# Optimization experiments

Hardware: AMD Instinct MI355X
Metric: run time of the kernel (lower is better)

Reference implementation:

```python
import jax, jax.numpy as jnp
import numpy as np

N, H, F, E, K = 4096, 512, 2048, 8, 2  # tokens, hidden, ffn(=4H), experts, top_k


def setup_inputs() -> dict:
    key = jax.random.key(0)
    ks = jax.random.split(key, 7)
    def w(k, shape, fan_in):
        return jax.random.normal(k, shape, dtype=jnp.float32) * (fan_in ** -0.5)
    return {
        "x": jax.random.normal(ks[0], (N, H), dtype=jnp.float32),
        "W_in": w(ks[1], (H, H), H),          # input_proj.weight  [out,in]
        "W_router": w(ks[2], (E, H), H),      # router.gate.weight [E,H]
        "W_gate": w(ks[3], (E, F, H), H),     # per-expert gate_proj.weight
        "W_up": w(ks[4], (E, F, H), H),       # per-expert up_proj.weight
        "W_down": w(ks[5], (E, H, F), F),     # per-expert down_proj.weight
        "W_out": w(ks[6], (H, H), H),         # output_proj.weight
    }


def reference(x, W_in, W_router, W_gate, W_up, W_down, W_out):
    h = x @ W_in.T                                  # [N,H] input_proj
    logits = h @ W_router.T                         # [N,E]
    # route_mode='balanced' and world_size==1 -> expert_bias is None
    probs = jax.nn.softmax(logits, axis=-1)
    top_w, top_i = jax.lax.top_k(probs, K)          # [N,K]
    top_w = jax.nn.softmax(top_w, axis=-1)          # renormalize over top-k

    # per-token combine weight for each expert: [N,E]
    onehot = jax.nn.one_hot(top_i, E, dtype=h.dtype)      # [N,K,E]
    combine_w = jnp.einsum('nk,nke->ne', top_w, onehot)

    def expert(wg, wu, wd):
        # SwiGLU FFN: down( silu(gate(h)) * up(h) )
        return (jax.nn.silu(h @ wg.T) * (h @ wu.T)) @ wd.T  # [N,H]

    expert_out = jax.vmap(expert)(W_gate, W_up, W_down)     # [E,N,H]
    combined = jnp.einsum('ne,enh->nh', combine_w, expert_out)
    return combined @ W_out.T                                # output_proj
```

## Files before the change

kernel.cpp:

```cpp
#include <hip/hip_runtime.h>
#include <hip/hip_bf16.h>

typedef unsigned short u16;
typedef unsigned int u32;
typedef short bf16x8 __attribute__((ext_vector_type(8)));
typedef float f32x4 __attribute__((ext_vector_type(4)));

#define AS1 __attribute__((address_space(1)))
#define AS3 __attribute__((address_space(3)))

#define NTOK 4096
#define HDIM 512
#define FDIM 2048
#define NEXP 8
#define NASSIGN (NTOK * 2)
#define NPAD (NASSIGN + NEXP * 128)
#define RBMAX 128

__device__ __forceinline__ void g2l16(const void* g, void* l) {
  __builtin_amdgcn_global_load_lds((const AS1 u32*)g, (AS3 u32*)l, 16, 0, 0);
}
__device__ __forceinline__ u16 f2bf(float f) {
  u32 u = __float_as_uint(f);
  u = (u + 0x7FFFu + ((u >> 16) & 1u)) >> 16;
  return (u16)u;
}
__device__ __forceinline__ float bf2f(u16 h) { return __uint_as_float(((u32)h) << 16); }
__device__ __forceinline__ u32 pkbf(float a, float b) {
  __hip_bfloat162 h = __float22bfloat162_rn(float2{a, b});
  u32 r;
  __builtin_memcpy(&r, &h, 4);
  return r;
}
__device__ __forceinline__ int4 pk8(const float4 a, const float4 b) {
  int4 r;
  r.x = (int)pkbf(a.x, a.y); r.y = (int)pkbf(a.z, a.w);
  r.z = (int)pkbf(b.x, b.y); r.w = (int)pkbf(b.z, b.w);
  return r;
}

#define WAITV6() asm volatile("s_waitcnt vmcnt(6)" ::: "memory")
#define WAITV4() asm volatile("s_waitcnt vmcnt(4)" ::: "memory")
#define WAITV2() asm volatile("s_waitcnt vmcnt(2)" ::: "memory")
#define WAITV0() asm volatile("s_waitcnt vmcnt(0)" ::: "memory")
#define LGKM0() asm volatile("s_waitcnt lgkmcnt(0)" ::: "memory")
#define BAR() __builtin_amdgcn_s_barrier()
#define SCB() __builtin_amdgcn_sched_barrier(0)
#define PRIO1() __builtin_amdgcn_s_setprio(1)
#define PRIO0() __builtin_amdgcn_s_setprio(0)
#define VMBAR() do { WAITV0(); BAR(); } while (0)

__global__ __launch_bounds__(256) void cvtall_kernel(
    const float* __restrict__ x, const float* __restrict__ Wi, const float* __restrict__ Wo,
    const float* __restrict__ Wg, const float* __restrict__ Wu, const float* __restrict__ Wd,
    u16* __restrict__ xb, u16* __restrict__ Wib, u16* __restrict__ Wob,
    u16* __restrict__ Wgb, u16* __restrict__ Wub, u16* __restrict__ Wdb) {
  const int c = blockIdx.x, tid = threadIdx.x;
  const float* s; u16* d; int cs;
  if (c < 128) { s = x; d = xb; cs = 0; }
  else if (c < 144) { s = Wi; d = Wib; cs = 128; }
  else if (c < 160) { s = Wo; d = Wob; cs = 144; }
  else if (c < 672) { s = Wg; d = Wgb; cs = 160; }
  else if (c < 1184) { s = Wu; d = Wub; cs = 672; }
  else { s = Wd; d = Wdb; cs = 1184; }
  const size_t base = (size_t)(c - cs) * 16384 + (size_t)tid * 8;
  const float* sp = s + base;
  u16* dp = d + base;
  float4 a[16];
#pragma unroll
  for (int j = 0; j < 8; ++j) {
    a[2 * j] = *(const float4*)(sp + j * 2048);
    a[2 * j + 1] = *(const float4*)(sp + j * 2048 + 4);
  }
#pragma unroll
  for (int j = 0; j < 8; ++j)
    *(int4*)(dp + j * 2048) = pk8(a[2 * j], a[2 * j + 1]);
}

__global__ __launch_bounds__(256) void wreff_kernel(
    const float* __restrict__ Wr, const float* __restrict__ Wi, double* __restrict__ wre) {
  const int t = blockIdx.x * 256 + threadIdx.x;
  const int e = t >> 9, k = t & 511;
  const float* wr = Wr + e * HDIM;
  double a0 = 0.0, a1 = 0.0, a2 = 0.0, a3 = 0.0;
  for (int j = 0; j < HDIM; j += 4) {
    a0 += (double)wr[j + 0] * (double)Wi[(j + 0) * HDIM + k];
    a1 += (double)wr[j + 1] * (double)Wi[(j + 1) * HDIM + k];
    a2 += (double)wr[j + 2] * (double)Wi[(j + 2) * HDIM + k];
    a3 += (double)wr[j + 3] * (double)Wi[(j + 3) * HDIM + k];
  }
  wre[t] = (a0 + a1) + (a2 + a3);
}

__global__ __launch_bounds__(128) void router_kernel(
    const float* __restrict__ x, const double* __restrict__ wre,
    int* __restrict__ idx, float* __restrict__ wts) {
  __shared__ double lw[NEXP * HDIM];
  for (int i = threadIdx.x; i < NEXP * HDIM; i += 128) lw[i] = wre[i];
  __syncthreads();
  const int n = blockIdx.x * 128 + threadIdx.x;
  const float* xr = x + (size_t)n * HDIM;
  double acc[NEXP] = {};
  for (int k4 = 0; k4 < HDIM / 4; ++k4) {
    const float4 xv = ((const float4*)xr)[k4];
    const float xc[4] = {xv.x, xv.y, xv.z, xv.w};
#pragma unroll
    for (int c = 0; c < 4; ++c) {
      const double xd = (double)xc[c];
#pragma unroll
      for (int e = 0; e < NEXP; ++e) acc[e] += xd * lw[e * HDIM + k4 * 4 + c];
    }
  }
  double mx = acc[0];
#pragma unroll
  for (int e = 1; e < NEXP; ++e) mx = acc[e] > mx ? acc[e] : mx;
  double p[NEXP], se = 0.0;
#pragma unroll
  for (int e = 0; e < NEXP; ++e) { p[e] = exp(acc[e] - mx); se += p[e]; }
  const double inv = 1.0 / se;
#pragma unroll
  for (int e = 0; e < NEXP; ++e) p[e] *= inv;
  int i0 = 0; double b0 = p[0];
#pragma unroll
  for (int e = 1; e < NEXP; ++e) if (p[e] > b0) { b0 = p[e]; i0 = e; }
  int i1 = -1; double b1 = -1.0;
#pragma unroll
  for (int e = 0; e < NEXP; ++e) if (e != i0 && p[e] > b1) { b1 = p[e]; i1 = e; }
  const double e0 = exp(b0), e1 = exp(b1);
  idx[2 * n] = i0; idx[2 * n + 1] = i1;
  wts[2 * n] = (float)(e0 / (e0 + e1));
  wts[2 * n + 1] = (float)(e1 / (e0 + e1));
}

__global__ void assign_kernel(const int* __restrict__ idx, int* __restrict__ tok,
                              int* __restrict__ pos, int* __restrict__ rbe,
                              int* __restrict__ rbp, int* __restrict__ nrb) {
  __shared__ int cnt[NEXP], cur[NEXP];
  const int tid = threadIdx.x;
  if (tid < NEXP) cnt[tid] = 0;
  __syncthreads();
  for (int a = tid; a < NASSIGN; a += 256) atomicAdd(&cnt[idx[a]], 1);
  __syncthreads();
  if (tid == 0) {
    int o = 0, n = 0;
    for (int e = 0; e < NEXP; ++e) {
      cur[e] = o;
      const int nb = (cnt[e] + 127) >> 7;
      for (int i = 0; i < nb; ++i) { rbe[n] = e; rbp[n] = o + i * 128; ++n; }
      o += nb * 128;
    }
    nrb[0] = n;
  }
  __syncthreads();
  for (int p = tid; p < NPAD; p += 256) tok[p] = 0;
  __syncthreads();
  for (int a = tid; a < NASSIGN; a += 256) {
    const int e = idx[a];
    const int q = atomicAdd(&cur[e], 1);
    tok[q] = a >> 1;
    pos[a] = q;
  }
}

template <int SB, int NT>
__device__ __forceinline__ void gemm128_body(
    const u16* __restrict__ A, const u16* __restrict__ B, void* __restrict__ C,
    int m0, int n0, int N, int K, u16* sm, int tid) {
  u16 *lA0 = sm, *lA1 = sm + 8192, *lB0 = sm + 16384, *lB1 = sm + 24576;
  const int w = tid >> 6, l = tid & 63;
  const int wm = (w >> 2) * 64, wn = (w & 3) * 32;
  const int lm = l & 15, lk = (l >> 4) * 8, xr = (l & 7) << 3;
  const int sr = l >> 3, sc = ((l & 7) ^ sr) * 8;
  const u16* As = A + (size_t)(m0 + w * 8 + sr) * K + sc;
  const u16* Bs = B + (size_t)(n0 + w * 8 + sr) * K + sc;
  f32x4 acc[4][2] = {};
  auto STG = [&](u16* dA, u16* dB, int kt) {
    g2l16(As + kt, dA + w * 512);
    g2l16(As + (size_t)64 * K + kt, dA + 4096 + w * 512);
    g2l16(Bs + kt, dB + w * 512);
    g2l16(Bs + (size_t)64 * K + kt, dB + 4096 + w * 512);
  };
  auto CMP = [&](const u16* a_, const u16* b_) {
#pragma unroll
    for (int kk = 0; kk < 2; ++kk) {
      const int ko = (kk * 32 + lk) ^ xr;
      bf16x8 af[4], bf[2];
#pragma unroll
      for (int i = 0; i < 4; ++i) af[i] = *(const bf16x8*)(a_ + (wm + i * 16 + lm) * 64 + ko);
#pragma unroll
      for (int j = 0; j < 2; ++j) bf[j] = *(const bf16x8*)(b_ + (wn + j * 16 + lm) * 64 + ko);
      PRIO1();
#pragma unroll
      for (int i = 0; i < 4; ++i)
#pragma unroll
        for (int j = 0; j < 2; ++j)
          acc[i][j] = __builtin_amdgcn_mfma_f32_16x16x32_bf16(af[i], bf[j], acc[i][j], 0, 0, 0);
      PRIO0();
    }
  };
  STG(lA0, lB0, 0);
  VMBAR();
  for (int t = 0; t < NT; t += 2) {
    if (t + 1 < NT) STG(lA1, lB1, (t + 1) * 64);
    CMP(lA0, lB0);
    VMBAR();
    if (t + 2 < NT) STG(lA0, lB0, (t + 2) * 64);
    CMP(lA1, lB1);
    VMBAR();
  }
  const int cr = (l >> 4) * 4, cc = lm;
#pragma unroll
  for (int i = 0; i < 4; ++i)
#pragma unroll
    for (int j = 0; j < 2; ++j)
#pragma unroll
      for (int r = 0; r < 4; ++r) {
        const size_t o = (size_t)(m0 + wm + i * 16 + cr + r) * N + n0 + wn + j * 16 + cc;
        if (SB) ((u16*)C)[o] = f2bf(acc[i][j][r]);
        else ((float*)C)[o] = acc[i][j][r];
      }
}

__global__ __launch_bounds__(512, 2) void ingemm_kernel(
    const u16* __restrict__ xb, const u16* __restrict__ Wib, u16* __restrict__ hb) {
  __shared__ __align__(16) u16 sm[32768];
  gemm128_body<1, 8>(xb, Wib, hb, blockIdx.y * 128, blockIdx.x * 128, HDIM, HDIM, sm, threadIdx.x);
}

__global__ __launch_bounds__(512, 2) void outgemm_kernel(
    const u16* __restrict__ dwn, const u16* __restrict__ Wob, const int* __restrict__ pos,
    const float* __restrict__ wts, float* __restrict__ out) {
  __shared__ __align__(16) u16 sm[32768];
  const int m0 = blockIdx.y * 128, n0 = blockIdx.x * 128;
  const int tid = threadIdx.x, w = tid >> 6, l = tid & 63;
  const int wm = (w >> 2) * 64, wn = (w & 3) * 32;
  const int lm = l & 15, lk = (l >> 4) * 8, xr = (l & 7) << 3;
  const int lr = l >> 3, c8 = l & 7;
  const int sc = (c8 ^ lr) * 8;
  const int t0 = m0 + w * 8 + lr, t1 = t0 + 64;
  const int p00 = pos[2 * t0], p01 = pos[2 * t0 + 1];
  const int p10 = pos[2 * t1], p11 = pos[2 * t1 + 1];
  const float w00 = wts[2 * t0], w01 = wts[2 * t0 + 1];
  const float w10 = wts[2 * t1], w11 = wts[2 * t1 + 1];
  const u16* A00 = dwn + (size_t)p00 * HDIM + c8 * 8;
  const u16* A01 = dwn + (size_t)p01 * HDIM + c8 * 8;
  const u16* A10 = dwn + (size_t)p10 * HDIM + c8 * 8;
  const u16* A11 = dwn + (size_t)p11 * HDIM + c8 * 8;
  const u16* Bs = Wob + (size_t)(n0 + w * 8 + lr) * HDIM + sc;
  f32x4 acc[4][2] = {};
  bf16x8 a00, a01, a10, a11;
  auto ALOAD = [&](int kt) {
    a00 = *(const bf16x8*)(A00 + kt); a01 = *(const bf16x8*)(A01 + kt);
    a10 = *(const bf16x8*)(A10 + kt); a11 = *(const bf16x8*)(A11 + kt);
  };
  auto AWRITE = [&](u16* st) {
    bf16x8 r0, r1;
#pragma unroll
    for (int q = 0; q < 8; ++q) {
      r0[q] = (short)f2bf(w00 * bf2f((u16)a00[q]) + w01 * bf2f((u16)a01[q]));
      r1[q] = (short)f2bf(w10 * bf2f((u16)a10[q]) + w11 * bf2f((u16)a11[q]));
    }
    *(bf16x8*)(st + (w * 8 + lr) * 64 + sc) = r0;
    *(bf16x8*)(st + (64 + w * 8 + lr) * 64 + sc) = r1;
  };
  auto STGB = [&](u16* st, int kt) {
    g2l16(Bs + kt, st + 8192 + w * 512);
    g2l16(Bs + (size_t)64 * HDIM + kt, st + 8192 + 4096 + w * 512);
  };
  auto CMP = [&](const u16* a_, const u16* b_) {
#pragma unroll
    for (int kk = 0; kk < 2; ++kk) {
      const int ko = (kk * 32 + lk) ^ xr;
      bf16x8 af[4], bf[2];
#pragma unroll
      for (int i = 0; i < 4; ++i) af[i] = *(const bf16x8*)(a_ + (wm + i * 16 + lm) * 64 + ko);
#pragma unroll
      for (int j = 0; j < 2; ++j) bf[j] = *(const bf16x8*)(b_ + (wn + j * 16 + lm) * 64 + ko);
      PRIO1();
#pragma unroll
      for (int i = 0; i < 4; ++i)
#pragma unroll
        for (int j = 0; j < 2; ++j)
          acc[i][j] = __builtin_amdgcn_mfma_f32_16x16x32_bf16(af[i], bf[j], acc[i][j], 0, 0, 0);
      PRIO0();
    }
  };
  ALOAD(0); SCB(); STGB(sm, 0);
  WAITV2(); AWRITE(sm);
  WAITV0(); LGKM0(); BAR(); SCB();
  for (int t = 0; t < 8; ++t) {
    u16* bu = sm + (t & 1) * 16384;
    u16* bn = sm + ((t + 1) & 1) * 16384;
    if (t < 7) { ALOAD((t + 1) * 64); SCB(); STGB(bn, (t + 1) * 64); }
    CMP(bu, bu + 8192);
    if (t < 7) { WAITV2(); AWRITE(bn); WAITV0(); }
    LGKM0(); BAR(); SCB();
  }
  const int cr = (l >> 4) * 4, cc = lm;
#pragma unroll
  for (int i = 0; i < 4; ++i)
#pragma unroll
    for (int j = 0; j < 2; ++j)
#pragma unroll
      for (int r = 0; r < 4; ++r)
        out[(size_t)(m0 + wm + i * 16 + cr + r) * HDIM + n0 + wn + j * 16 + cc] = acc[i][j][r];
}

__global__ __launch_bounds__(512, 2) void gateup_kernel(
    const u16* __restrict__ hb, const u16* __restrict__ Wg, const u16* __restrict__ Wu,
    u16* __restrict__ act, const int* __restrict__ tok, const int* __restrict__ rbe,
    const int* __restrict__ rbp, const int* __restrict__ nrb) {
  const int rb = blockIdx.y;
  if (rb >= nrb[0]) return;
  __shared__ __align__(16) u16 sm[73728];
  const int e = rbe[rb], p0 = rbp[rb], n0 = blockIdx.x * 128;
  const int tid = threadIdx.x, w = tid >> 6, l = tid & 63;
  const int wm = (w >> 2) * 64, wn = (w & 3) * 32;
  const int lm = l & 15, lk = (l >> 4) * 8, xr = (l & 7) << 3;
  const int sr = l >> 3, sc = ((l & 7) ^ sr) * 8;
  const u16* A0 = hb + (size_t)tok[p0 + w * 8 + sr] * HDIM + sc;
  const u16* A1 = hb + (size_t)tok[p0 + 64 + w * 8 + sr] * HDIM + sc;
  const u16* G0 = Wg + (size_t)e * FDIM * HDIM + (size_t)(n0 + w * 8 + sr) * HDIM + sc;
  const u16* G1 = G0 + (size_t)64 * HDIM;
  const u16* U0 = Wu + (size_t)e * FDIM * HDIM + (size_t)(n0 + w * 8 + sr) * HDIM + sc;
  const u16* U1 = U0 + (size_t)64 * HDIM;
  f32x4 ag[4][2] = {}, au[4][2] = {};
  auto STG = [&](int b, int kt) {
    u16* d = sm + b * 24576;
    g2l16(A0 + kt, d + w * 512);
    g2l16(A1 + kt, d + 4096 + w * 512);
    g2l16(G0 + kt, d + 8192 + w * 512);
    g2l16(G1 + kt, d + 12288 + w * 512);
    g2l16(U0 + kt, d + 16384 + w * 512);
    g2l16(U1 + kt, d + 20480 + w * 512);
  };
  auto CMP = [&](int b) {
    const u16* a_ = sm + b * 24576;
    const u16* g_ = a_ + 8192;
    const u16* u_ = a_ + 16384;
#pragma unroll
    for (int kk = 0; kk < 2; ++kk) {
      const int ko = (kk * 32 + lk) ^ xr;
      bf16x8 af[4], gf[2], uf[2];
#pragma unroll
      for (int i = 0; i < 4; ++i) af[i] = *(const bf16x8*)(a_ + (wm + i * 16 + lm) * 64 + ko);
#pragma unroll
      for (int j = 0; j < 2; ++j) {
        gf[j] = *(const bf16x8*)(g_ + (wn + j * 16 + lm) * 64 + ko);
        uf[j] = *(const bf16x8*)(u_ + (wn + j * 16 + lm) * 64 + ko);
      }
#pragma unroll
      for (int i = 0; i < 4; ++i)
#pragma unroll
        for (int j = 0; j < 2; ++j) {
          ag[i][j] = __builtin_amdgcn_mfma_f32_16x16x32_bf16(af[i], gf[j], ag[i][j], 0, 0, 0);
          au[i][j] = __builtin_amdgcn_mfma_f32_16x16x32_bf16(af[i], uf[j], au[i][j], 0, 0, 0);
        }
    }
  };
  STG(0, 0); STG(1, 64);
  WAITV6(); BAR();
#pragma unroll
  for (int t = 0; t < 8; ++t) {
    if (t + 2 < 8) STG((t + 2) % 3, (t + 2) * 64);
    CMP(t % 3);
    if (t + 2 < 8) WAITV6(); else WAITV0();
    BAR();
  }
  const int cr = (l >> 4) * 4, cc = lm;
#pragma unroll
  for (int i = 0; i < 4; ++i)
#pragma unroll
    for (int j = 0; j < 2; ++j)
#pragma unroll
      for (int r = 0; r < 4; ++r) {
        const float g = ag[i][j][r], u = au[i][j][r];
        const float s = g / (1.0f + __expf(-g));
        act[(size_t)(p0 + wm + i * 16 + cr + r) * FDIM + n0 + wn + j * 16 + cc] = f2bf(s * u);
      }
}

__global__ __launch_bounds__(512, 2) void down_kernel(
    const u16* __restrict__ act, const u16* __restrict__ Wd, u16* __restrict__ dwn,
    const int* __restrict__ rbe, const int* __restrict__ rbp, const int* __restrict__ nrb) {
  const int rb = blockIdx.y;
  if (rb >= nrb[0]) return;
  __shared__ __align__(16) u16 sm[49152];
  const int e = rbe[rb], p0 = rbp[rb], n0 = blockIdx.x * 128;
  const int tid = threadIdx.x, w = tid >> 6, l = tid & 63;
  const int g = w >> 2;
  const int wm = ((w >> 1) & 1) * 64, wn = (w & 1) * 64;
  const int lm = l & 15, lk = (l >> 4) * 8, xr = (l & 7) << 3;
  const int ko = (g * 32 + lk) ^ xr;
  const int sr = l >> 3, sc = ((l & 7) ^ sr) * 8;
  const u16* As = act + (size_t)(p0 + w * 8 + sr) * FDIM + sc;
  const u16* Bs = Wd + (size_t)e * HDIM * FDIM + (size_t)(n0 + w * 8 + sr) * FDIM + sc;
  f32x4 acc[4][4] = {};
  auto STG = [&](int b, int kt) {
    u16* d = sm + b * 16384;
    g2l16(As + kt, d + w * 512);
    g2l16(As + (size_t)64 * FDIM + kt, d + 4096 + w * 512);
    g2l16(Bs + kt, d + 8192 + w * 512);
    g2l16(Bs + (size_t)64 * FDIM + kt, d + 12288 + w * 512);
  };
  auto CMP = [&](int b) {
    const u16* a_ = sm + b * 16384;
    const u16* b_ = a_ + 8192;
    bf16x8 af[4], bf[4];
#pragma unroll
    for (int i = 0; i < 4; ++i) af[i] = *(const bf16x8*)(a_ + (wm + i * 16 + lm) * 64 + ko);
#pragma unroll
    for (int j = 0; j < 4; ++j) bf[j] = *(const bf16x8*)(b_ + (wn + j * 16 + lm) * 64 + ko);
#pragma unroll
    for (int i = 0; i < 4; ++i)
#pragma unroll
      for (int j = 0; j < 4; ++j)
        acc[i][j] = __builtin_amdgcn_mfma_f32_16x16x32_bf16(af[i], bf[j], acc[i][j], 0, 0, 0);
  };
  STG(0, 0); STG(1, 64);
  WAITV4(); BAR();
#pragma unroll
  for (int t = 0; t < 32; ++t) {
    if (t + 2 < 32) STG((t + 2) % 3, (t + 2) * 64);
    CMP(t % 3);
    if (t + 2 < 32) WAITV4(); else WAITV0();
    BAR();
  }
  LGKM0();
  SCB();
  BAR();
  float* red = (float*)sm;
  if (g == 1) {
#pragma unroll
    for (int i = 0; i < 4; ++i)
#pragma unroll
      for (int j = 0; j < 4; ++j)
        *(f32x4*)&red[(w & 3) * 4096 + (i * 4 + j) * 256 + l * 4] = acc[i][j];
  }
  BAR();
  if (g == 0) {
    const int cr = (l >> 4) * 4, cc = lm;
#pragma unroll
    for (int i = 0; i < 4; ++i)
#pragma unroll
      for (int j = 0; j < 4; ++j) {
        const f32x4 o = *(const f32x4*)&red[w * 4096 + (i * 4 + j) * 256 + l * 4];
        const f32x4 s = acc[i][j] + o;
#pragma unroll
        for (int r = 0; r < 4; ++r)
          dwn[(size_t)(p0 + wm + i * 16 + cr + r) * HDIM + n0 + wn + j * 16 + cc] = f2bf(s[r]);
      }
  }
}

extern "C" void kernel_launch(void* const* d_in, const int* in_sizes, int n_in,
                              void* d_out, int out_size, void* d_ws, size_t ws_size,
                              hipStream_t stream) {
  const float* x  = (const float*)d_in[0];
  const float* Wi = (const float*)d_in[1];
  const float* Wr = (const float*)d_in[2];
  const float* Wg = (const float*)d_in[3];
  const float* Wu = (const float*)d_in[4];
  const float* Wd = (const float*)d_in[5];
  const float* Wo = (const float*)d_in[6];
  float* out = (float*)d_out;

  char* ws = (char*)d_ws;
  size_t off = 0;
  auto alloc = [&](size_t bytes) -> void* {
    off = (off + 255) & ~(size_t)255;
    void* p = ws + off;
    off += bytes;
    return p;
  };
  u16* xb   = (u16*)alloc((size_t)NTOK * HDIM * 2);
  u16* hb   = (u16*)alloc((size_t)NTOK * HDIM * 2);
  u16* Wib  = (u16*)alloc((size_t)HDIM * HDIM * 2);
  u16* Wob  = (u16*)alloc((size_t)HDIM * HDIM * 2);
  u16* Wgb  = (u16*)alloc((size_t)NEXP * FDIM * HDIM * 2);
  u16* Wub  = (u16*)alloc((size_t)NEXP * FDIM * HDIM * 2);
  u16* Wdb  = (u16*)alloc((size_t)NEXP * HDIM * FDIM * 2);
  u16* actb = (u16*)alloc((size_t)NPAD * FDIM * 2);
  u16* dwn  = (u16*)alloc((size_t)NPAD * HDIM * 2);
  double* wre = (double*)alloc((size_t)NEXP * HDIM * 8);
  int* idx = (int*)alloc((size_t)NASSIGN * 4);
  float* wts = (float*)alloc((size_t)NASSIGN * 4);
  int* tok = (int*)alloc((size_t)NPAD * 4);
  int* pos = (int*)alloc((size_t)NASSIGN * 4);
  int* rbe = (int*)alloc((size_t)RBMAX * 4);
  int* rbp = (int*)alloc((size_t)RBMAX * 4);
  int* nrb = (int*)alloc(256);

  cvtall_kernel<<<1696, 256, 0, stream>>>(x, Wi, Wo, Wg, Wu, Wd, xb, Wib, Wob, Wgb, Wub, Wdb);
  wreff_kernel<<<16, 256, 0, stream>>>(Wr, Wi, wre);
  router_kernel<<<32, 128, 0, stream>>>(x, wre, idx, wts);
  assign_kernel<<<1, 256, 0, stream>>>(idx, tok, pos, rbe, rbp, nrb);
  ingemm_kernel<<<dim3(4, 32), 512, 0, stream>>>(xb, Wib, hb);
  gateup_kernel<<<dim3(16, 72), 512, 0, stream>>>(hb, Wgb, Wub, actb, tok, rbe, rbp, nrb);
  down_kernel<<<dim3(4, 72), 512, 0, stream>>>(actb, Wdb, dwn, rbe, rbp, nrb);
  outgemm_kernel<<<dim3(4, 32), 512, 0, stream>>>(dwn, Wob, pos, wts, out);
}
```

Before: 226.6 us.

## Enlarge gate/up expert tiles to 256 rows and split combine into separate kernel

```diff
diff --git a/kernel.cpp b/kernel.cpp
--- a/kernel.cpp
+++ b/kernel.cpp
@@ -14,7 +14,7 @@
 #define FDIM 2048
 #define NEXP 8
 #define NASSIGN (NTOK * 2)
-#define NPAD (NASSIGN + NEXP * 128)
+#define NPAD2 (NASSIGN + NEXP * 256)
 #define RBMAX 128
 
 __device__ __forceinline__ void g2l16(const void* g, void* l) {
@@ -39,9 +39,7 @@
   return r;
 }
 
-#define WAITV6() asm volatile("s_waitcnt vmcnt(6)" ::: "memory")
 #define WAITV4() asm volatile("s_waitcnt vmcnt(4)" ::: "memory")
-#define WAITV2() asm volatile("s_waitcnt vmcnt(2)" ::: "memory")
 #define WAITV0() asm volatile("s_waitcnt vmcnt(0)" ::: "memory")
 #define LGKM0() asm volatile("s_waitcnt lgkmcnt(0)" ::: "memory")
 #define BAR() __builtin_amdgcn_s_barrier()
@@ -133,8 +131,9 @@
 }
 
 __global__ void assign_kernel(const int* __restrict__ idx, int* __restrict__ tok,
-                              int* __restrict__ pos, int* __restrict__ rbe,
-                              int* __restrict__ rbp, int* __restrict__ nrb) {
+                              int* __restrict__ pos, int* __restrict__ rbe2,
+                              int* __restrict__ rbp2, int* __restrict__ rbe1,
+                              int* __restrict__ rbp1, int* __restrict__ nrb) {
   __shared__ int cnt[NEXP], cur[NEXP];
   const int tid = threadIdx.x;
   if (tid < NEXP) cnt[tid] = 0;
@@ -142,17 +141,19 @@
   for (int a = tid; a < NASSIGN; a += 256) atomicAdd(&cnt[idx[a]], 1);
   __syncthreads();
   if (tid == 0) {
-    int o = 0, n = 0;
+    int o = 0, n2 = 0, n1 = 0;
     for (int e = 0; e < NEXP; ++e) {
       cur[e] = o;
-      const int nb = (cnt[e] + 127) >> 7;
-      for (int i = 0; i < nb; ++i) { rbe[n] = e; rbp[n] = o + i * 128; ++n; }
-      o += nb * 128;
+      const int nb2 = (cnt[e] + 255) >> 8;
+      const int nb1 = (cnt[e] + 127) >> 7;
+      for (int i = 0; i < nb2; ++i) { rbe2[n2] = e; rbp2[n2] = o + i * 256; ++n2; }
+      for (int i = 0; i < nb1; ++i) { rbe1[n1] = e; rbp1[n1] = o + i * 128; ++n1; }
+      o += nb2 * 256;
     }
-    nrb[0] = n;
+    nrb[0] = n2; nrb[1] = n1;
   }
   __syncthreads();
-  for (int p = tid; p < NPAD; p += 256) tok[p] = 0;
+  for (int p = tid; p < NPAD2; p += 256) tok[p] = 0;
   __syncthreads();
   for (int a = tid; a < NASSIGN; a += 256) {
     const int e = idx[a];
@@ -228,165 +229,109 @@
 }
 
 __global__ __launch_bounds__(512, 2) void outgemm_kernel(
-    const u16* __restrict__ dwn, const u16* __restrict__ Wob, const int* __restrict__ pos,
-    const float* __restrict__ wts, float* __restrict__ out) {
+    const u16* __restrict__ cb, const u16* __restrict__ Wob, float* __restrict__ out) {
   __shared__ __align__(16) u16 sm[32768];
-  const int m0 = blockIdx.y * 128, n0 = blockIdx.x * 128;
+  gemm128_body<0, 8>(cb, Wob, out, blockIdx.y * 128, blockIdx.x * 128, HDIM, HDIM, sm, threadIdx.x);
+}
+
+__global__ __launch_bounds__(512, 2) void gateup_kernel(
+    const u16* __restrict__ hb, const u16* __restrict__ Wg, const u16* __restrict__ Wu,
+    u16* __restrict__ act, const int* __restrict__ tok, const int* __restrict__ rbe2,
+    const int* __restrict__ rbp2, const int* __restrict__ nrb) {
+  const int rb = blockIdx.y;
+  if (rb >= nrb[0]) return;
+  __shared__ __align__(16) u16 sm[65536];
+  const int e = rbe2[rb], p0 = rbp2[rb], n0 = blockIdx.x * 128;
   const int tid = threadIdx.x, w = tid >> 6, l = tid & 63;
-  const int wm = (w >> 2) * 64, wn = (w & 3) * 32;
+  const int half = w >> 2, rh = (w >> 1) & 1, ch = w & 1;
   const int lm = l & 15, lk = (l >> 4) * 8, xr = (l & 7) << 3;
-  const int lr = l >> 3, c8 = l & 7;
-  const int sc = (c8 ^ lr) * 8;
-  const int t0 = m0 + w * 8 + lr, t1 = t0 + 64;
-  const int p00 = pos[2 * t0], p01 = pos[2 * t0 + 1];
-  const int p10 = pos[2 * t1], p11 = pos[2 * t1 + 1];
-  const float w00 = wts[2 * t0], w01 = wts[2 * t0 + 1];
-  const float w10 = wts[2 * t1], w11 = wts[2 * t1 + 1];
-  const u16* A00 = dwn + (size_t)p00 * HDIM + c8 * 8;
-  const u16* A01 = dwn + (size_t)p01 * HDIM + c8 * 8;
-  const u16* A10 = dwn + (size_t)p10 * HDIM + c8 * 8;
-  const u16* A11 = dwn + (size_t)p11 * HDIM + c8 * 8;
-  const u16* Bs = Wob + (size_t)(n0 + w * 8 + lr) * HDIM + sc;
-  f32x4 acc[4][2] = {};
-  bf16x8 a00, a01, a10, a11;
-  auto ALOAD = [&](int kt) {
-    a00 = *(const bf16x8*)(A00 + kt); a01 = *(const bf16x8*)(A01 + kt);
-    a10 = *(const bf16x8*)(A10 + kt); a11 = *(const bf16x8*)(A11 + kt);
-  };
-  auto AWRITE = [&](u16* st) {
-    bf16x8 r0, r1;
-#pragma unroll
-    for (int q = 0; q < 8; ++q) {
-      r0[q] = (short)f2bf(w00 * bf2f((u16)a00[q]) + w01 * bf2f((u16)a01[q]));
-      r1[q] = (short)f2bf(w10 * bf2f((u16)a10[q]) + w11 * bf2f((u16)a11[q]));
+  const int sr = l >> 3, sc = ((l & 7) ^ sr) * 8;
+  const u16* Asrc[4];
+#pragma unroll
+  for (int c = 0; c < 4; ++c)
+    Asrc[c] = hb + (size_t)tok[p0 + c * 64 + w * 8 + sr] * HDIM + sc;
+  const u16 *Gsrc[2], *Usrc[2];
+#pragma unroll
+  for (int c = 0; c < 2; ++c) {
+    Gsrc[c] = Wg + (size_t)e * FDIM * HDIM + (size_t)(n0 + c * 64 + w * 8 + sr) * HDIM + sc;
+    Usrc[c] = Wu + (size_t)e * FDIM * HDIM + (size_t)(n0 + c * 64 + w * 8 + sr) * HDIM + sc;
+  }
+  f32x4 acc[8][4] = {};
+  auto STG = [&](int b, int kt) {
+    u16* d = sm + b * 32768;
+#pragma unroll
+    for (int c = 0; c < 4; ++c) g2l16(Asrc[c] + kt, d + c * 4096 + w * 512);
+#pragma unroll
+    for (int c = 0; c < 2; ++c) {
+      g2l16(Gsrc[c] + kt, d + 16384 + c * 4096 + w * 512);
+      g2l16(Usrc[c] + kt, d + 24576 + c * 4096 + w * 512);
     }
-    *(bf16x8*)(st + (w * 8 + lr) * 64 + sc) = r0;
-    *(bf16x8*)(st + (64 + w * 8 + lr) * 64 + sc) = r1;
-  };
-  auto STGB = [&](u16* st, int kt) {
-    g2l16(Bs + kt, st + 8192 + w * 512);
-    g2l16(Bs + (size_t)64 * HDIM + kt, st + 8192 + 4096 + w * 512);
-  };
-  auto CMP = [&](const u16* a_, const u16* b_) {
+  };
+  auto CMP = [&](int b) {
+    const u16* A_ = sm + b * 32768;
+    const u16* B_ = A_ + 16384 + half * 8192;
 #pragma unroll
     for (int kk = 0; kk < 2; ++kk) {
       const int ko = (kk * 32 + lk) ^ xr;
-      bf16x8 af[4], bf[2];
-#pragma unroll
-      for (int i = 0; i < 4; ++i) af[i] = *(const bf16x8*)(a_ + (wm + i * 16 + lm) * 64 + ko);
-#pragma unroll
-      for (int j = 0; j < 2; ++j) bf[j] = *(const bf16x8*)(b_ + (wn + j * 16 + lm) * 64 + ko);
+      bf16x8 af[8], bf[4];
+#pragma unroll
+      for (int i = 0; i < 8; ++i)
+        af[i] = *(const bf16x8*)(A_ + (rh * 128 + i * 16 + lm) * 64 + ko);
+#pragma unroll
+      for (int j = 0; j < 4; ++j)
+        bf[j] = *(const bf16x8*)(B_ + (ch * 64 + j * 16 + lm) * 64 + ko);
       PRIO1();
 #pragma unroll
-      for (int i = 0; i < 4; ++i)
-#pragma unroll
-        for (int j = 0; j < 2; ++j)
+      for (int i = 0; i < 8; ++i)
+#pragma unroll
+        for (int j = 0; j < 4; ++j)
           acc[i][j] = __builtin_amdgcn_mfma_f32_16x16x32_bf16(af[i], bf[j], acc[i][j], 0, 0, 0);
       PRIO0();
     }
   };
-  ALOAD(0); SCB(); STGB(sm, 0);
-  WAITV2(); AWRITE(sm);
-  WAITV0(); LGKM0(); BAR(); SCB();
+  STG(0, 0);
+  VMBAR();
+#pragma unroll
   for (int t = 0; t < 8; ++t) {
-    u16* bu = sm + (t & 1) * 16384;
-    u16* bn = sm + ((t + 1) & 1) * 16384;
-    if (t < 7) { ALOAD((t + 1) * 64); SCB(); STGB(bn, (t + 1) * 64); }
-    CMP(bu, bu + 8192);
-    if (t < 7) { WAITV2(); AWRITE(bn); WAITV0(); }
-    LGKM0(); BAR(); SCB();
+    if (t < 7) STG((t + 1) & 1, (t + 1) * 64);
+    CMP(t & 1);
+    VMBAR();
   }
   const int cr = (l >> 4) * 4, cc = lm;
-#pragma unroll
-  for (int i = 0; i < 4; ++i)
-#pragma unroll
-    for (int j = 0; j < 2; ++j)
-#pragma unroll
-      for (int r = 0; r < 4; ++r)
-        out[(size_t)(m0 + wm + i * 16 + cr + r) * HDIM + n0 + wn + j * 16 + cc] = acc[i][j][r];
-}
-
-__global__ __launch_bounds__(512, 2) void gateup_kernel(
-    const u16* __restrict__ hb, const u16* __restrict__ Wg, const u16* __restrict__ Wu,
-    u16* __restrict__ act, const int* __restrict__ tok, const int* __restrict__ rbe,
-    const int* __restrict__ rbp, const int* __restrict__ nrb) {
-  const int rb = blockIdx.y;
-  if (rb >= nrb[0]) return;
-  __shared__ __align__(16) u16 sm[73728];
-  const int e = rbe[rb], p0 = rbp[rb], n0 = blockIdx.x * 128;
-  const int tid = threadIdx.x, w = tid >> 6, l = tid & 63;
-  const int wm = (w >> 2) * 64, wn = (w & 3) * 32;
-  const int lm = l & 15, lk = (l >> 4) * 8, xr = (l & 7) << 3;
-  const int sr = l >> 3, sc = ((l & 7) ^ sr) * 8;
-  const u16* A0 = hb + (size_t)tok[p0 + w * 8 + sr] * HDIM + sc;
-  const u16* A1 = hb + (size_t)tok[p0 + 64 + w * 8 + sr] * HDIM + sc;
-  const u16* G0 = Wg + (size_t)e * FDIM * HDIM + (size_t)(n0 + w * 8 + sr) * HDIM + sc;
-  const u16* G1 = G0 + (size_t)64 * HDIM;
-  const u16* U0 = Wu + (size_t)e * FDIM * HDIM + (size_t)(n0 + w * 8 + sr) * HDIM + sc;
-  const u16* U1 = U0 + (size_t)64 * HDIM;
-  f32x4 ag[4][2] = {}, au[4][2] = {};
-  auto STG = [&](int b, int kt) {
-    u16* d = sm + b * 24576;
-    g2l16(A0 + kt, d + w * 512);
-    g2l16(A1 + kt, d + 4096 + w * 512);
-    g2l16(G0 + kt, d + 8192 + w * 512);
-    g2l16(G1 + kt, d + 12288 + w * 512);
-    g2l16(U0 + kt, d + 16384 + w * 512);
-    g2l16(U1 + kt, d + 20480 + w * 512);
-  };
-  auto CMP = [&](int b) {
-    const u16* a_ = sm + b * 24576;
-    const u16* g_ = a_ + 8192;
-    const u16* u_ = a_ + 16384;
-#pragma unroll
-    for (int kk = 0; kk < 2; ++kk) {
-      const int ko = (kk * 32 + lk) ^ xr;
-      bf16x8 af[4], gf[2], uf[2];
-#pragma unroll
-      for (int i = 0; i < 4; ++i) af[i] = *(const bf16x8*)(a_ + (wm + i * 16 + lm) * 64 + ko);
-#pragma unroll
-      for (int j = 0; j < 2; ++j) {
-        gf[j] = *(const bf16x8*)(g_ + (wn + j * 16 + lm) * 64 + ko);
-        uf[j] = *(const bf16x8*)(u_ + (wn + j * 16 + lm) * 64 + ko);
+  float* red = (float*)sm;
+  if (half == 1) {
+#pragma unroll
+    for (int i = 0; i < 8; ++i)
+#pragma unroll
+      for (int j = 0; j < 4; ++j)
+        *(f32x4*)&red[(w - 4) * 8192 + (i * 4 + j) * 256 + l * 4] = acc[i][j];
+  }
+  LGKM0();
+  BAR();
+  if (half == 0) {
+#pragma unroll
+    for (int i = 0; i < 8; ++i)
+#pragma unroll
+      for (int j = 0; j < 4; ++j) {
+        const f32x4 ua = *(const f32x4*)&red[w * 8192 + (i * 4 + j) * 256 + l * 4];
+#pragma unroll
+        for (int r = 0; r < 4; ++r) {
+          const float g = acc[i][j][r], u = ua[r];
+          const float s = g / (1.0f + __expf(-g));
+          act[(size_t)(p0 + rh * 128 + i * 16 + cr + r) * FDIM + n0 + ch * 64 + j * 16 + cc] =
+              f2bf(s * u);
+        }
       }
-#pragma unroll
-      for (int i = 0; i < 4; ++i)
-#pragma unroll
-        for (int j = 0; j < 2; ++j) {
-          ag[i][j] = __builtin_amdgcn_mfma_f32_16x16x32_bf16(af[i], gf[j], ag[i][j], 0, 0, 0);
-          au[i][j] = __builtin_amdgcn_mfma_f32_16x16x32_bf16(af[i], uf[j], au[i][j], 0, 0, 0);
-        }
-    }
-  };
-  STG(0, 0); STG(1, 64);
-  WAITV6(); BAR();
-#pragma unroll
-  for (int t = 0; t < 8; ++t) {
-    if (t + 2 < 8) STG((t + 2) % 3, (t + 2) * 64);
-    CMP(t % 3);
-    if (t + 2 < 8) WAITV6(); else WAITV0();
-    BAR();
-  }
-  const int cr = (l >> 4) * 4, cc = lm;
-#pragma unroll
-  for (int i = 0; i < 4; ++i)
-#pragma unroll
-    for (int j = 0; j < 2; ++j)
-#pragma unroll
-      for (int r = 0; r < 4; ++r) {
-        const float g = ag[i][j][r], u = au[i][j][r];
-        const float s = g / (1.0f + __expf(-g));
-        act[(size_t)(p0 + wm + i * 16 + cr + r) * FDIM + n0 + wn + j * 16 + cc] = f2bf(s * u);
-      }
+  }
 }
 
 __global__ __launch_bounds__(512, 2) void down_kernel(
     const u16* __restrict__ act, const u16* __restrict__ Wd, u16* __restrict__ dwn,
-    const int* __restrict__ rbe, const int* __restrict__ rbp, const int* __restrict__ nrb) {
+    const int* __restrict__ rbe1, const int* __restrict__ rbp1, const int* __restrict__ nrb) {
   const int rb = blockIdx.y;
-  if (rb >= nrb[0]) return;
+  if (rb >= nrb[1]) return;
   __shared__ __align__(16) u16 sm[49152];
-  const int e = rbe[rb], p0 = rbp[rb], n0 = blockIdx.x * 128;
+  const int e = rbe1[rb], p0 = rbp1[rb], n0 = blockIdx.x * 128;
   const int tid = threadIdx.x, w = tid >> 6, l = tid & 63;
   const int g = w >> 2;
   const int wm = ((w >> 1) & 1) * 64, wn = (w & 1) * 64;
@@ -453,6 +398,21 @@
   }
 }
 
+__global__ void combine_kernel(const u16* __restrict__ dwn, const int* __restrict__ pos,
+                               const float* __restrict__ wts, u16* __restrict__ cb) {
+  const int n = blockIdx.x, t = threadIdx.x;
+  const int p0 = pos[2 * n], p1 = pos[2 * n + 1];
+  const float w0 = wts[2 * n], w1 = wts[2 * n + 1];
+  const ushort4 a = ((const ushort4*)(dwn + (size_t)p0 * HDIM))[t];
+  const ushort4 b = ((const ushort4*)(dwn + (size_t)p1 * HDIM))[t];
+  ushort4 o;
+  o.x = f2bf(w0 * bf2f(a.x) + w1 * bf2f(b.x));
+  o.y = f2bf(w0 * bf2f(a.y) + w1 * bf2f(b.y));
+  o.z = f2bf(w0 * bf2f(a.z) + w1 * bf2f(b.z));
+  o.w = f2bf(w0 * bf2f(a.w) + w1 * bf2f(b.w));
+  ((ushort4*)(cb + (size_t)n * HDIM))[t] = o;
+}
+
 extern "C" void kernel_launch(void* const* d_in, const int* in_sizes, int n_in,
                               void* d_out, int out_size, void* d_ws, size_t ws_size,
                               hipStream_t stream) {
@@ -475,28 +435,32 @@
   };
   u16* xb   = (u16*)alloc((size_t)NTOK * HDIM * 2);
   u16* hb   = (u16*)alloc((size_t)NTOK * HDIM * 2);
+  u16* cb   = (u16*)alloc((size_t)NTOK * HDIM * 2);
   u16* Wib  = (u16*)alloc((size_t)HDIM * HDIM * 2);
   u16* Wob  = (u16*)alloc((size_t)HDIM * HDIM * 2);
   u16* Wgb  = (u16*)alloc((size_t)NEXP * FDIM * HDIM * 2);
   u16* Wub  = (u16*)alloc((size_t)NEXP * FDIM * HDIM * 2);
   u16* Wdb  = (u16*)alloc((size_t)NEXP * HDIM * FDIM * 2);
-  u16* actb = (u16*)alloc((size_t)NPAD * FDIM * 2);
-  u16* dwn  = (u16*)alloc((size_t)NPAD * HDIM * 2);
+  u16* actb = (u16*)alloc((size_t)NPAD2 * FDIM * 2);
+  u16* dwn  = (u16*)alloc((size_t)NPAD2 * HDIM * 2);
   double* wre = (double*)alloc((size_t)NEXP * HDIM * 8);
   int* idx = (int*)alloc((size_t)NASSIGN * 4);
   float* wts = (float*)alloc((size_t)NASSIGN * 4);
-  int* tok = (int*)alloc((size_t)NPAD * 4);
+  int* tok = (int*)alloc((size_t)NPAD2 * 4);
   int* pos = (int*)alloc((size_t)NASSIGN * 4);
-  int* rbe = (int*)alloc((size_t)RBMAX * 4);
-  int* rbp = (int*)alloc((size_t)RBMAX * 4);
+  int* rbe2 = (int*)alloc((size_t)RBMAX * 4);
+  int* rbp2 = (int*)alloc((size_t)RBMAX * 4);
+  int* rbe1 = (int*)alloc((size_t)RBMAX * 4);
+  int* rbp1 = (int*)alloc((size_t)RBMAX * 4);
   int* nrb = (int*)alloc(256);
 
   cvtall_kernel<<<1696, 256, 0, stream>>>(x, Wi, Wo, Wg, Wu, Wd, xb, Wib, Wob, Wgb, Wub, Wdb);
   wreff_kernel<<<16, 256, 0, stream>>>(Wr, Wi, wre);
   router_kernel<<<32, 128, 0, stream>>>(x, wre, idx, wts);
-  assign_kernel<<<1, 256, 0, stream>>>(idx, tok, pos, rbe, rbp, nrb);
+  assign_kernel<<<1, 256, 0, stream>>>(idx, tok, pos, rbe2, rbp2, rbe1, rbp1, nrb);
   ingemm_kernel<<<dim3(4, 32), 512, 0, stream>>>(xb, Wib, hb);
-  gateup_kernel<<<dim3(16, 72), 512, 0, stream>>>(hb, Wgb, Wub, actb, tok, rbe, rbp, nrb);
-  down_kernel<<<dim3(4, 72), 512, 0, stream>>>(actb, Wdb, dwn, rbe, rbp, nrb);
-  outgemm_kernel<<<dim3(4, 32), 512, 0, stream>>>(dwn, Wob, pos, wts, out);
-}
+  gateup_kernel<<<dim3(16, 40), 512, 0, stream>>>(hb, Wgb, Wub, actb, tok, rbe2, rbp2, nrb);
+  down_kernel<<<dim3(4, 72), 512, 0, stream>>>(actb, Wdb, dwn, rbe1, rbp1, nrb);
+  combine_kernel<<<NTOK, 128, 0, stream>>>(dwn, pos, wts, cb);
+  outgemm_kernel<<<dim3(4, 32), 512, 0, stream>>>(cb, Wob, out);
+}
```

Measured after the change: 235.2 us. +3.8%, slower.
